# Performance work log

Hardware: AMD Instinct MI355X
Metric: run time of the kernel (lower is better)

The kernel has to match this reference:

```python
import jax, jax.numpy as jnp
import numpy as np

N, E = 50000, 1600000
IN_CH, HEADS, OUT_PER_HEAD = 128, 4, 32  # out_channels=128 // 4 heads
NEG_SLOPE = 0.2


def setup_inputs() -> dict:
    key = jax.random.key(0)
    ks = jax.random.split(key, 10)
    HC = HEADS * OUT_PER_HEAD
    glorot = lambda k, shape: jax.random.uniform(k, shape, jnp.float32, -1.0, 1.0) * jnp.sqrt(6.0 / (shape[0] + shape[-1]))
    return {
        "x": jax.random.normal(ks[0], (N, IN_CH), jnp.float32),
        "edge_index": jax.random.randint(ks[1], (2, E), 0, N),
        "edge_weight": jax.random.uniform(ks[2], (E,), jnp.float32),
        "Wl": glorot(ks[3], (IN_CH, HC)),
        "bl": jnp.zeros((HC,), jnp.float32),
        "Wr": glorot(ks[4], (IN_CH, HC)),
        "br": jnp.zeros((HC,), jnp.float32),
        "We": glorot(ks[5], (1, HC)),           # lin_edge, bias=False
        "att": glorot(ks[6], (HEADS, OUT_PER_HEAD)),
        "bias": jnp.zeros((HC,), jnp.float32),
    }


def reference(x, edge_index, edge_weight, Wl, bl, Wr, br, We, att, bias):
    n = x.shape[0]
    H, C = att.shape
    src, dst = edge_index[0], edge_index[1]
    # add_self_loops with fill_value='max': self-loop edge_attr = max incoming edge weight per node (0 if none)
    loop_attr = jax.ops.segment_max(edge_weight, dst, num_segments=n)
    loop_attr = jnp.where(jnp.isfinite(loop_attr), loop_attr, 0.0)
    loop = jnp.arange(n)
    src_f = jnp.concatenate([src, loop])
    dst_f = jnp.concatenate([dst, loop])
    ea_f = jnp.concatenate([edge_weight, loop_attr])[:, None]  # [E+N, 1]
    # GATv2: separate src/dst linear transforms
    x_l = (x @ Wl + bl).reshape(n, H, C)
    x_r = (x @ Wr + br).reshape(n, H, C)
    e = (ea_f @ We).reshape(-1, H, C)
    # per-edge message and attention score
    m = jax.nn.leaky_relu(x_l[src_f] + x_r[dst_f] + e, NEG_SLOPE)  # [E+N, H, C]
    alpha = jnp.einsum('ehc,hc->eh', m, att)
    # scatter-softmax over incoming edges per destination node
    amax = jax.ops.segment_max(alpha, dst_f, num_segments=n)
    amax = jnp.where(jnp.isfinite(amax), amax, 0.0)
    aexp = jnp.exp(alpha - amax[dst_f])
    asum = jax.ops.segment_sum(aexp, dst_f, num_segments=n)
    alpha = aexp / (asum[dst_f] + 1e-16)
    # weighted aggregate of source-transformed features
    out = jax.ops.segment_sum(x_l[src_f] * alpha[..., None], dst_f, num_segments=n)
    return out.reshape(n, H * C) + bias
```

## Files before the change

kernel.cpp:

```cpp
#include <hip/hip_runtime.h>
#include <cstdint>

#define NEG 0.2f
#define BSH 4
#define BNODES 16
#define CAP 768
#define EPT 3
#define SBSH 9
#define SBN 512
#define CCAP 18000
#define CCHUNK 3328
#define CEPT 13
#define LOG2E 1.44269504088896f

typedef __attribute__((ext_vector_type(8))) short short8v;
typedef __attribute__((ext_vector_type(4))) float f32x4;

__device__ __forceinline__ unsigned short f2bf(float f) {
  unsigned u = __float_as_uint(f);
  return (unsigned short)((u + 0x7FFFu + ((u >> 16) & 1u)) >> 16);
}

__global__ __launch_bounds__(256) void k_prep(const float* __restrict__ Wl,
    const float* __restrict__ Wr, unsigned short* __restrict__ WtB) {
  int mat = blockIdx.x;
  const float* W = mat ? Wr : Wl;
  for (int i = threadIdx.x; i < 16384; i += 256) {
    int c = i >> 7, k = i & 127;
    WtB[mat * 16384 + c * 128 + k] = f2bf(W[k * 128 + c]);
  }
}

__global__ __launch_bounds__(256) void k_gemm(const float* __restrict__ x,
    const unsigned short* __restrict__ WtB,
    const float* __restrict__ bl, const float* __restrict__ br,
    unsigned short* __restrict__ xlb, unsigned short* __restrict__ xrb, int n) {
  __shared__ __align__(16) unsigned short xs[64][136];
  __shared__ __align__(16) unsigned short Wt[128][136];
  int tid = threadIdx.x;
  int B0 = blockIdx.x * 64;
  int mat = blockIdx.y;
  for (int i = tid; i < 64 * 32; i += 256) {
    int r = i >> 5, c4 = (i & 31) * 4;
    ushort4 o = {0, 0, 0, 0};
    if (B0 + r < n) {
      float4 v = *(const float4*)(x + (size_t)(B0 + r) * 128 + c4);
      o = make_ushort4(f2bf(v.x), f2bf(v.y), f2bf(v.z), f2bf(v.w));
    }
    *(ushort4*)&xs[r][c4] = o;
  }
  for (int i = tid; i < 128 * 32; i += 256) {
    int c = i >> 5, k4 = (i & 31) * 4;
    *(ushort4*)&Wt[c][k4] = *(const ushort4*)(WtB + (size_t)mat * 16384 + c * 128 + k4);
  }
  __syncthreads();
  int wv = tid >> 6, lane = tid & 63;
  int l15 = lane & 15, g = lane >> 4;
  int R0 = wv * 16;
  f32x4 acc[8];
  #pragma unroll
  for (int t = 0; t < 8; ++t) acc[t] = {0.f, 0.f, 0.f, 0.f};
  #pragma unroll
  for (int kc = 0; kc < 4; ++kc) {
    int k0 = kc * 32 + g * 8;
    short8v b = *(const short8v*)&xs[R0 + l15][k0];
    #pragma unroll
    for (int t = 0; t < 8; ++t) {
      short8v a = *(const short8v*)&Wt[t * 16 + l15][k0];
      acc[t] = __builtin_amdgcn_mfma_f32_16x16x32_bf16(a, b, acc[t], 0, 0, 0);
    }
  }
  const float* bias = mat ? br : bl;
  unsigned short* yp = mat ? xrb : xlb;
  int row = B0 + R0 + l15;
  if (row < n) {
    #pragma unroll
    for (int t = 0; t < 8; ++t) {
      int c0 = t * 16 + g * 4;
      float4 bv = *(const float4*)(bias + c0);
      ushort4 o = {f2bf(acc[t][0] + bv.x), f2bf(acc[t][1] + bv.y),
                   f2bf(acc[t][2] + bv.z), f2bf(acc[t][3] + bv.w)};
      *(ushort4*)(yp + (size_t)row * 128 + c0) = o;
    }
  }
}

__global__ __launch_bounds__(256) void k_coarse(const int* __restrict__ eidx,
    const float* __restrict__ ew, unsigned* __restrict__ gsb,
    int2* __restrict__ csb, int E, int NSB) {
  __shared__ unsigned cnt[128];
  __shared__ unsigned base[128];
  int c0 = blockIdx.x * CCHUNK;
  int c1 = min(E, c0 + CCHUNK);
  if (c0 >= c1) return;
  for (int b = threadIdx.x; b < NSB; b += 256) cnt[b] = 0u;
  __syncthreads();
  unsigned dreg[CEPT];
  #pragma unroll
  for (int k = 0; k < CEPT; ++k) {
    int i = c0 + threadIdx.x + k * 256;
    unsigned d = 0u;
    if (i < c1) {
      d = (unsigned)eidx[E + i];
      atomicAdd(&cnt[d >> SBSH], 1u);
    }
    dreg[k] = d;
  }
  __syncthreads();
  for (int b = threadIdx.x; b < NSB; b += 256) {
    unsigned c = cnt[b];
    base[b] = c ? atomicAdd(&gsb[b], c) : 0u;
    cnt[b] = 0u;
  }
  __syncthreads();
  #pragma unroll
  for (int k = 0; k < CEPT; ++k) {
    int i = c0 + threadIdx.x + k * 256;
    if (i < c1) {
      unsigned d = dreg[k];
      unsigned b = d >> SBSH;
      unsigned slot = base[b] + atomicAdd(&cnt[b], 1u);
      if (slot < CCAP)
        csb[(size_t)b * CCAP + slot] =
            make_int2((eidx[i] << SBSH) | (int)(d & (SBN - 1)), __float_as_int(ew[i]));
    }
  }
}

__global__ __launch_bounds__(1024) void k_fine(const unsigned* __restrict__ gsb,
    const int2* __restrict__ csb, int2* __restrict__ ebkt,
    unsigned* __restrict__ fcnt, int NB) {
  __shared__ unsigned cnt[32];
  int sb = blockIdx.x;
  int ne = min((int)gsb[sb], CCAP);
  const int2* src = csb + (size_t)sb * CCAP;
  if (threadIdx.x < 32) cnt[threadIdx.x] = 0u;
  __syncthreads();
  for (int i = threadIdx.x; i < ne; i += 1024) {
    int2 e = src[i];
    int fb = (e.x >> 4) & 31;
    unsigned slot = atomicAdd(&cnt[fb], 1u);
    if (slot < CAP) {
      int packed = ((e.x >> SBSH) << 4) | (e.x & 15);
      ebkt[(size_t)(sb * 32 + fb) * CAP + slot] = make_int2(packed, e.y);
    }
  }
  __syncthreads();
  if (threadIdx.x < 32) {
    int fb = sb * 32 + (int)threadIdx.x;
    if (fb < NB) fcnt[fb] = min(cnt[threadIdx.x], (unsigned)CAP);
  }
}

__global__ __launch_bounds__(256) void k_agg(
    const unsigned* __restrict__ fcnt, const int2* __restrict__ ebkt,
    const unsigned short* __restrict__ xlb, const unsigned short* __restrict__ xrb,
    const float* __restrict__ We, const float* __restrict__ att,
    const float* __restrict__ bias, float* __restrict__ out, int n) {
  __shared__ int2 es[CAP];
  __shared__ unsigned rp[BNODES + 1];
  __shared__ unsigned cur[BNODES];
  __shared__ unsigned scnt[BNODES];
  int tid = threadIdx.x;
  int lane = tid & 63, wv = tid >> 6;
  int bkt = blockIdx.x;
  int ne = min((int)fcnt[bkt], CAP);
  const int2* srcp = ebkt + (size_t)bkt * CAP;
  if (tid < BNODES) scnt[tid] = 0u;
  __syncthreads();
  int2 er[EPT];
  #pragma unroll
  for (int k = 0; k < EPT; ++k) {
    int i = tid + k * 256;
    if (i < ne) {
      er[k] = srcp[i];
      atomicAdd(&scnt[er[k].x & (BNODES - 1)], 1u);
    }
  }
  __syncthreads();
  if (tid < 64) {
    unsigned s = (lane < BNODES) ? scnt[lane] : 0u;
    #pragma unroll
    for (int off = 1; off < BNODES; off <<= 1) {
      unsigned t = __shfl_up(s, off);
      if (lane >= off) s += t;
    }
    if (lane < BNODES) { rp[lane + 1] = s; cur[lane] = 0u; }
    if (lane == 0) rp[0] = 0u;
  }
  __syncthreads();
  #pragma unroll
  for (int k = 0; k < EPT; ++k) {
    int i = tid + k * 256;
    if (i < ne) {
      int dl = er[k].x & (BNODES - 1);
      unsigned slot = rp[dl] + atomicAdd(&cur[dl], 1u);
      es[slot] = make_int2(er[k].x >> BSH, er[k].y);
    }
  }
  __syncthreads();

  int g = lane >> 4;
  int l4 = lane & 15;
  int ch0 = l4 * 8;
  float4 weA = *(const float4*)(We + ch0);
  float4 weB = *(const float4*)(We + ch0 + 4);
  float4 atA = *(const float4*)(att + ch0);
  float4 atB = *(const float4*)(att + ch0 + 4);
  atA.x *= LOG2E; atA.y *= LOG2E; atA.z *= LOG2E; atA.w *= LOG2E;
  atB.x *= LOG2E; atB.y *= LOG2E; atB.z *= LOG2E; atB.w *= LOG2E;

  for (int dl = wv; dl < BNODES; dl += 4) {
    int d = (bkt << BSH) + dl;
    if (d >= n) break;
    int s0 = (int)rp[dl], s1 = (int)rp[dl + 1];
    uint4 xrq = *(const uint4*)(xrb + ((size_t)d << 7) + ch0);
    float4 xrA, xrB;
    xrA.x = __uint_as_float(xrq.x << 16);
    xrA.y = __uint_as_float(xrq.x & 0xFFFF0000u);
    xrA.z = __uint_as_float(xrq.y << 16);
    xrA.w = __uint_as_float(xrq.y & 0xFFFF0000u);
    xrB.x = __uint_as_float(xrq.z << 16);
    xrB.y = __uint_as_float(xrq.z & 0xFFFF0000u);
    xrB.z = __uint_as_float(xrq.w << 16);
    xrB.w = __uint_as_float(xrq.w & 0xFFFF0000u);
    float den = 0.f, wmax = -INFINITY;
    float4 aA = {0, 0, 0, 0}, aB = {0, 0, 0, 0};
    int idx = s0 + g;
    bool valid = idx < s1;
    int2 ev = make_int2(0, 0);
    uint4 xq = {0, 0, 0, 0};
    if (valid) {
      ev = es[idx];
      xq = *(const uint4*)(xlb + ((size_t)ev.x << 7) + ch0);
    }
    for (int j = s0; j < s1; j += 4) {
      int idxn = j + 4 + g;
      bool vn = idxn < s1;
      int2 evn = ev; uint4 xqn = xq;
      if (vn) {
        evn = es[idxn];
        xqn = *(const uint4*)(xlb + ((size_t)evn.x << 7) + ch0);
      }
      if (valid) {
        float w = __int_as_float(ev.y);
        wmax = fmaxf(wmax, w);
        float4 xA, xB;
        xA.x = __uint_as_float(xq.x << 16);
        xA.y = __uint_as_float(xq.x & 0xFFFF0000u);
        xA.z = __uint_as_float(xq.y << 16);
        xA.w = __uint_as_float(xq.y & 0xFFFF0000u);
        xB.x = __uint_as_float(xq.z << 16);
        xB.y = __uint_as_float(xq.z & 0xFFFF0000u);
        xB.z = __uint_as_float(xq.w << 16);
        xB.w = __uint_as_float(xq.w & 0xFFFF0000u);
        float4 tA, tB;
        tA.x = xA.x + xrA.x + w * weA.x;
        tA.y = xA.y + xrA.y + w * weA.y;
        tA.z = xA.z + xrA.z + w * weA.z;
        tA.w = xA.w + xrA.w + w * weA.w;
        tB.x = xB.x + xrB.x + w * weB.x;
        tB.y = xB.y + xrB.y + w * weB.y;
        tB.z = xB.z + xrB.z + w * weB.z;
        tB.w = xB.w + xrB.w + w * weB.w;
        tA.x = fmaxf(tA.x, NEG * tA.x);
        tA.y = fmaxf(tA.y, NEG * tA.y);
        tA.z = fmaxf(tA.z, NEG * tA.z);
        tA.w = fmaxf(tA.w, NEG * tA.w);
        tB.x = fmaxf(tB.x, NEG * tB.x);
        tB.y = fmaxf(tB.y, NEG * tB.y);
        tB.z = fmaxf(tB.z, NEG * tB.z);
        tB.w = fmaxf(tB.w, NEG * tB.w);
        float p = tA.x * atA.x + tA.y * atA.y + tA.z * atA.z + tA.w * atA.w
                + tB.x * atB.x + tB.y * atB.y + tB.z * atB.z + tB.w * atB.w;
        p += __shfl_xor(p, 1);
        p += __shfl_xor(p, 2);
        float pe = exp2f(p);
        den += pe;
        aA.x += pe * xA.x; aA.y += pe * xA.y; aA.z += pe * xA.z; aA.w += pe * xA.w;
        aB.x += pe * xB.x; aB.y += pe * xB.y; aB.z += pe * xB.z; aB.w += pe * xB.w;
      }
      ev = evn; xq = xqn; valid = vn;
    }
    #pragma unroll
    for (int mask = 16; mask <= 32; mask <<= 1) {
      den += __shfl_xor(den, mask);
      aA.x += __shfl_xor(aA.x, mask); aA.y += __shfl_xor(aA.y, mask);
      aA.z += __shfl_xor(aA.z, mask); aA.w += __shfl_xor(aA.w, mask);
      aB.x += __shfl_xor(aB.x, mask); aB.y += __shfl_xor(aB.y, mask);
      aB.z += __shfl_xor(aB.z, mask); aB.w += __shfl_xor(aB.w, mask);
      wmax = fmaxf(wmax, __shfl_xor(wmax, mask));
    }
    {
      float wl = (wmax > -INFINITY) ? wmax : 0.f;
      uint4 xq2 = *(const uint4*)(xlb + ((size_t)d << 7) + ch0);
      float4 xA, xB;
      xA.x = __uint_as_float(xq2.x << 16);
      xA.y = __uint_as_float(xq2.x & 0xFFFF0000u);
      xA.z = __uint_as_float(xq2.y << 16);
      xA.w = __uint_as_float(xq2.y & 0xFFFF0000u);
      xB.x = __uint_as_float(xq2.z << 16);
      xB.y = __uint_as_float(xq2.z & 0xFFFF0000u);
      xB.z = __uint_as_float(xq2.w << 16);
      xB.w = __uint_as_float(xq2.w & 0xFFFF0000u);
      float4 tA, tB;
      tA.x = xA.x + xrA.x + wl * weA.x;
      tA.y = xA.y + xrA.y + wl * weA.y;
      tA.z = xA.z + xrA.z + wl * weA.z;
      tA.w = xA.w + xrA.w + wl * weA.w;
      tB.x = xB.x + xrB.x + wl * weB.x;
      tB.y = xB.y + xrB.y + wl * weB.y;
      tB.z = xB.z + xrB.z + wl * weB.z;
      tB.w = xB.w + xrB.w + wl * weB.w;
      tA.x = fmaxf(tA.x, NEG * tA.x);
      tA.y = fmaxf(tA.y, NEG * tA.y);
      tA.z = fmaxf(tA.z, NEG * tA.z);
      tA.w = fmaxf(tA.w, NEG * tA.w);
      tB.x = fmaxf(tB.x, NEG * tB.x);
      tB.y = fmaxf(tB.y, NEG * tB.y);
      tB.z = fmaxf(tB.z, NEG * tB.z);
      tB.w = fmaxf(tB.w, NEG * tB.w);
      float p = tA.x * atA.x + tA.y * atA.y + tA.z * atA.z + tA.w * atA.w
              + tB.x * atB.x + tB.y * atB.y + tB.z * atB.z + tB.w * atB.w;
      p += __shfl_xor(p, 1);
      p += __shfl_xor(p, 2);
      float pe = exp2f(p);
      den += pe;
      aA.x += pe * xA.x; aA.y += pe * xA.y; aA.z += pe * xA.z; aA.w += pe * xA.w;
      aB.x += pe * xB.x; aB.y += pe * xB.y; aB.z += pe * xB.z; aB.w += pe * xB.w;
    }
    if (g == 0) {
      float r = 1.0f / den;
      float4 bvA = *(const float4*)(bias + ch0);
      float4 bvB = *(const float4*)(bias + ch0 + 4);
      float* op = out + (size_t)d * 128 + ch0;
      float4 oA = {aA.x * r + bvA.x, aA.y * r + bvA.y, aA.z * r + bvA.z, aA.w * r + bvA.w};
      float4 oB = {aB.x * r + bvB.x, aB.y * r + bvB.y, aB.z * r + bvB.z, aB.w * r + bvB.w};
      *(float4*)op = oA;
      *(float4*)(op + 4) = oB;
    }
  }
}

extern "C" void kernel_launch(void* const* d_in, const int* in_sizes, int n_in,
                              void* d_out, int out_size, void* d_ws, size_t ws_size,
                              hipStream_t stream) {
  const float* x     = (const float*)d_in[0];
  const int*   eidx  = (const int*)d_in[1];
  const float* ew_in = (const float*)d_in[2];
  const float* Wl    = (const float*)d_in[3];
  const float* bl    = (const float*)d_in[4];
  const float* Wr    = (const float*)d_in[5];
  const float* br    = (const float*)d_in[6];
  const float* We    = (const float*)d_in[7];
  const float* att   = (const float*)d_in[8];
  const float* bias  = (const float*)d_in[9];
  float* out = (float*)d_out;

  const int N = in_sizes[0] / 128;
  const int E = in_sizes[2];
  const int NB = (N + BNODES - 1) >> BSH;
  const int NSB = (N + SBN - 1) >> SBSH;

  char* ws = (char*)d_ws;
  size_t off = 0;
  auto alloc = [&](size_t bytes) {
    void* p = ws + off;
    off = (off + bytes + 255) & ~(size_t)255;
    return p;
  };
  int2* ebkt = (int2*)alloc((size_t)NB * CAP * 8);
  size_t ov_start = off;
  unsigned short* xlb = (unsigned short*)alloc((size_t)N * 128 * 2);
  unsigned short* xrb = (unsigned short*)alloc((size_t)N * 128 * 2);
  int2* csb = (int2*)(ws + ov_start);
  unsigned short* WtB = (unsigned short*)alloc(2 * 16384 * 2);
  unsigned* fcnt = (unsigned*)alloc((size_t)NB * 4);
  unsigned* gsb  = (unsigned*)alloc((size_t)NSB * 4);

  hipMemsetAsync(gsb, 0, (size_t)NSB * 4, stream);

  k_prep<<<2, 256, 0, stream>>>(Wl, Wr, WtB);

  int nblk = (E + CCHUNK - 1) / CCHUNK;
  k_coarse<<<nblk, 256, 0, stream>>>(eidx, ew_in, gsb, csb, E, NSB);

  k_fine<<<NSB, 1024, 0, stream>>>(gsb, csb, ebkt, fcnt, NB);

  k_gemm<<<dim3((N + 63) / 64, 2), 256, 0, stream>>>(x, WtB, bl, br, xlb, xrb, N);

  k_agg<<<NB, 256, 0, stream>>>(fcnt, ebkt, xlb, xrb, We, att, bias, out, N);
}
```

Baseline: 165.3 us.

## Decompose leaky-relu attention into linear terms plus abs and split fine bucketing

Rewrites leaky_relu(t)·att as 0.6·att·t + 0.4·att·|t|. The linear part is precomputed per node in the GEMM epilogue (ql, qr) and per head for the edge weight (qe), so the per-edge loop only needs an fma+abs chain instead of max and multiply. Separately, k_fine is split into 8 slices per super-bucket using two-pass counting with global atomic bases to raise parallelism. Costs are extra per-node scalar loads and memsetting fcnt, plus small numerical differences because the linear part is computed from bf16-rounded features.

Measured after the change: 162.6 us. No clear change (-1.7%).

```diff
diff --git a/kernel.cpp b/kernel.cpp
--- a/kernel.cpp
+++ b/kernel.cpp
@@ -11,6 +11,7 @@
 #define CCAP 18000
 #define CCHUNK 3328
 #define CEPT 13
+#define FSLICE 8
 #define LOG2E 1.44269504088896f
 
 typedef __attribute__((ext_vector_type(8))) short short8v;
@@ -20,21 +21,37 @@
   unsigned u = __float_as_uint(f);
   return (unsigned short)((u + 0x7FFFu + ((u >> 16) & 1u)) >> 16);
 }
+__device__ __forceinline__ float bf2f(unsigned short h) {
+  return __uint_as_float(((unsigned)h) << 16);
+}
 
 __global__ __launch_bounds__(256) void k_prep(const float* __restrict__ Wl,
-    const float* __restrict__ Wr, unsigned short* __restrict__ WtB) {
+    const float* __restrict__ Wr, const float* __restrict__ We,
+    const float* __restrict__ att, unsigned short* __restrict__ WtB,
+    float* __restrict__ qe) {
   int mat = blockIdx.x;
   const float* W = mat ? Wr : Wl;
   for (int i = threadIdx.x; i < 16384; i += 256) {
     int c = i >> 7, k = i & 127;
     WtB[mat * 16384 + c * 128 + k] = f2bf(W[k * 128 + c]);
   }
+  if (mat == 0) {
+    __shared__ float tmp[128];
+    if (threadIdx.x < 128) tmp[threadIdx.x] = att[threadIdx.x] * We[threadIdx.x];
+    __syncthreads();
+    if (threadIdx.x < 4) {
+      float s = 0.f;
+      for (int c = 0; c < 32; ++c) s += tmp[threadIdx.x * 32 + c];
+      qe[threadIdx.x] = 0.6f * LOG2E * s;
+    }
+  }
 }
 
 __global__ __launch_bounds__(256) void k_gemm(const float* __restrict__ x,
-    const unsigned short* __restrict__ WtB,
+    const unsigned short* __restrict__ WtB, const float* __restrict__ att,
     const float* __restrict__ bl, const float* __restrict__ br,
-    unsigned short* __restrict__ xlb, unsigned short* __restrict__ xrb, int n) {
+    unsigned short* __restrict__ xlb, unsigned short* __restrict__ xrb,
+    float* __restrict__ ql, float* __restrict__ qr, int n) {
   __shared__ __align__(16) unsigned short xs[64][136];
   __shared__ __align__(16) unsigned short Wt[128][136];
   int tid = threadIdx.x;
@@ -72,17 +89,31 @@
   }
   const float* bias = mat ? br : bl;
   unsigned short* yp = mat ? xrb : xlb;
+  float* qdst = mat ? qr : ql;
   int row = B0 + R0 + l15;
+  float qp[4] = {0.f, 0.f, 0.f, 0.f};
   if (row < n) {
+    const float s06 = 0.6f * LOG2E;
     #pragma unroll
     for (int t = 0; t < 8; ++t) {
       int c0 = t * 16 + g * 4;
       float4 bv = *(const float4*)(bias + c0);
+      float4 av = *(const float4*)(att + c0);
       ushort4 o = {f2bf(acc[t][0] + bv.x), f2bf(acc[t][1] + bv.y),
                    f2bf(acc[t][2] + bv.z), f2bf(acc[t][3] + bv.w)};
       *(ushort4*)(yp + (size_t)row * 128 + c0) = o;
-    }
-  }
+      float dot = av.x * bf2f(o.x) + av.y * bf2f(o.y)
+                + av.z * bf2f(o.z) + av.w * bf2f(o.w);
+      qp[t >> 1] += s06 * dot;
+    }
+  }
+  #pragma unroll
+  for (int h = 0; h < 4; ++h) {
+    qp[h] += __shfl_xor(qp[h], 16);
+    qp[h] += __shfl_xor(qp[h], 32);
+  }
+  if (row < n && g == 0)
+    *(float4*)(qdst + (size_t)row * 4) = make_float4(qp[0], qp[1], qp[2], qp[3]);
 }
 
 __global__ __launch_bounds__(256) void k_coarse(const int* __restrict__ eidx,
@@ -127,36 +158,47 @@
   }
 }
 
-__global__ __launch_bounds__(1024) void k_fine(const unsigned* __restrict__ gsb,
+__global__ __launch_bounds__(256) void k_fine(const unsigned* __restrict__ gsb,
     const int2* __restrict__ csb, int2* __restrict__ ebkt,
     unsigned* __restrict__ fcnt, int NB) {
   __shared__ unsigned cnt[32];
-  int sb = blockIdx.x;
+  __shared__ unsigned base[32];
+  int sb = blockIdx.x / FSLICE;
+  int sl = blockIdx.x % FSLICE;
   int ne = min((int)gsb[sb], CCAP);
+  int chunk = (ne + FSLICE - 1) / FSLICE;
+  int i0 = sl * chunk, i1 = min(ne, i0 + chunk);
+  if (i0 >= i1) return;
   const int2* src = csb + (size_t)sb * CCAP;
   if (threadIdx.x < 32) cnt[threadIdx.x] = 0u;
   __syncthreads();
-  for (int i = threadIdx.x; i < ne; i += 1024) {
+  for (int i = i0 + threadIdx.x; i < i1; i += 256)
+    atomicAdd(&cnt[(src[i].x >> 4) & 31], 1u);
+  __syncthreads();
+  if (threadIdx.x < 32) {
+    unsigned c = cnt[threadIdx.x];
+    base[threadIdx.x] = c ? atomicAdd(&fcnt[sb * 32 + (int)threadIdx.x], c) : 0u;
+    cnt[threadIdx.x] = 0u;
+  }
+  __syncthreads();
+  for (int i = i0 + threadIdx.x; i < i1; i += 256) {
     int2 e = src[i];
     int fb = (e.x >> 4) & 31;
-    unsigned slot = atomicAdd(&cnt[fb], 1u);
+    unsigned slot = base[fb] + atomicAdd(&cnt[fb], 1u);
     if (slot < CAP) {
       int packed = ((e.x >> SBSH) << 4) | (e.x & 15);
       ebkt[(size_t)(sb * 32 + fb) * CAP + slot] = make_int2(packed, e.y);
     }
   }
-  __syncthreads();
-  if (threadIdx.x < 32) {
-    int fb = sb * 32 + (int)threadIdx.x;
-    if (fb < NB) fcnt[fb] = min(cnt[threadIdx.x], (unsigned)CAP);
-  }
 }
 
 __global__ __launch_bounds__(256) void k_agg(
     const unsigned* __restrict__ fcnt, const int2* __restrict__ ebkt,
     const unsigned short* __restrict__ xlb, const unsigned short* __restrict__ xrb,
-    const float* __restrict__ We, const float* __restrict__ att,
-    const float* __restrict__ bias, float* __restrict__ out, int n) {
+    const float* __restrict__ ql, const float* __restrict__ qr,
+    const float* __restrict__ qe, const float* __restrict__ We,
+    const float* __restrict__ att, const float* __restrict__ bias,
+    float* __restrict__ out, int n) {
   __shared__ int2 es[CAP];
   __shared__ unsigned rp[BNODES + 1];
   __shared__ unsigned cur[BNODES];
@@ -202,13 +244,16 @@
 
   int g = lane >> 4;
   int l4 = lane & 15;
+  int h = l4 >> 2;
   int ch0 = l4 * 8;
   float4 weA = *(const float4*)(We + ch0);
   float4 weB = *(const float4*)(We + ch0 + 4);
   float4 atA = *(const float4*)(att + ch0);
   float4 atB = *(const float4*)(att + ch0 + 4);
-  atA.x *= LOG2E; atA.y *= LOG2E; atA.z *= LOG2E; atA.w *= LOG2E;
-  atB.x *= LOG2E; atB.y *= LOG2E; atB.z *= LOG2E; atB.w *= LOG2E;
+  const float s04 = 0.4f * LOG2E;
+  atA.x *= s04; atA.y *= s04; atA.z *= s04; atA.w *= s04;
+  atB.x *= s04; atB.y *= s04; atB.z *= s04; atB.w *= s04;
+  float qeh = qe[h];
 
   for (int dl = wv; dl < BNODES; dl += 4) {
     int d = (bkt << BSH) + dl;
@@ -224,23 +269,27 @@
     xrB.y = __uint_as_float(xrq.z & 0xFFFF0000u);
     xrB.z = __uint_as_float(xrq.w << 16);
     xrB.w = __uint_as_float(xrq.w & 0xFFFF0000u);
+    float qrd = qr[(size_t)d * 4 + h];
     float den = 0.f, wmax = -INFINITY;
     float4 aA = {0, 0, 0, 0}, aB = {0, 0, 0, 0};
     int idx = s0 + g;
     bool valid = idx < s1;
     int2 ev = make_int2(0, 0);
     uint4 xq = {0, 0, 0, 0};
+    float qls = 0.f;
     if (valid) {
       ev = es[idx];
       xq = *(const uint4*)(xlb + ((size_t)ev.x << 7) + ch0);
+      qls = ql[(size_t)ev.x * 4 + h];
     }
     for (int j = s0; j < s1; j += 4) {
       int idxn = j + 4 + g;
       bool vn = idxn < s1;
-      int2 evn = ev; uint4 xqn = xq;
+      int2 evn = ev; uint4 xqn = xq; float qln = qls;
       if (vn) {
         evn = es[idxn];
         xqn = *(const uint4*)(xlb + ((size_t)evn.x << 7) + ch0);
+        qln = ql[(size_t)evn.x * 4 + h];
       }
       if (valid) {
         float w = __int_as_float(ev.y);
@@ -254,33 +303,23 @@
         xB.y = __uint_as_float(xq.z & 0xFFFF0000u);
         xB.z = __uint_as_float(xq.w << 16);
         xB.w = __uint_as_float(xq.w & 0xFFFF0000u);
-        float4 tA, tB;
-        tA.x = xA.x + xrA.x + w * weA.x;
-        tA.y = xA.y + xrA.y + w * weA.y;
-        tA.z = xA.z + xrA.z + w * weA.z;
-        tA.w = xA.w + xrA.w + w * weA.w;
-        tB.x = xB.x + xrB.x + w * weB.x;
-        tB.y = xB.y + xrB.y + w * weB.y;
-        tB.z = xB.z + xrB.z + w * weB.z;
-        tB.w = xB.w + xrB.w + w * weB.w;
-        tA.x = fmaxf(tA.x, NEG * tA.x);
-        tA.y = fmaxf(tA.y, NEG * tA.y);
-        tA.z = fmaxf(tA.z, NEG * tA.z);
-        tA.w = fmaxf(tA.w, NEG * tA.w);
-        tB.x = fmaxf(tB.x, NEG * tB.x);
-        tB.y = fmaxf(tB.y, NEG * tB.y);
-        tB.z = fmaxf(tB.z, NEG * tB.z);
-        tB.w = fmaxf(tB.w, NEG * tB.w);
-        float p = tA.x * atA.x + tA.y * atA.y + tA.z * atA.z + tA.w * atA.w
-                + tB.x * atB.x + tB.y * atB.y + tB.z * atB.z + tB.w * atB.w;
-        p += __shfl_xor(p, 1);
-        p += __shfl_xor(p, 2);
-        float pe = exp2f(p);
+        float nl = 0.f, t;
+        t = xA.x + fmaf(w, weA.x, xrA.x); nl = fmaf(atA.x, fabsf(t), nl);
+        t = xA.y + fmaf(w, weA.y, xrA.y); nl = fmaf(atA.y, fabsf(t), nl);
+        t = xA.z + fmaf(w, weA.z, xrA.z); nl = fmaf(atA.z, fabsf(t), nl);
+        t = xA.w + fmaf(w, weA.w, xrA.w); nl = fmaf(atA.w, fabsf(t), nl);
+        t = xB.x + fmaf(w, weB.x, xrB.x); nl = fmaf(atB.x, fabsf(t), nl);
+        t = xB.y + fmaf(w, weB.y, xrB.y); nl = fmaf(atB.y, fabsf(t), nl);
+        t = xB.z + fmaf(w, weB.z, xrB.z); nl = fmaf(atB.z, fabsf(t), nl);
+        t = xB.w + fmaf(w, weB.w, xrB.w); nl = fmaf(atB.w, fabsf(t), nl);
+        nl += __shfl_xor(nl, 1);
+        nl += __shfl_xor(nl, 2);
+        float pe = exp2f(qls + fmaf(w, qeh, qrd) + nl);
         den += pe;
         aA.x += pe * xA.x; aA.y += pe * xA.y; aA.z += pe * xA.z; aA.w += pe * xA.w;
         aB.x += pe * xB.x; aB.y += pe * xB.y; aB.z += pe * xB.z; aB.w += pe * xB.w;
       }
-      ev = evn; xq = xqn; valid = vn;
+      ev = evn; xq = xqn; qls = qln; valid = vn;
     }
     #pragma unroll
     for (int mask = 16; mask <= 32; mask <<= 1) {
@@ -303,28 +342,19 @@
       xB.y = __uint_as_float(xq2.z & 0xFFFF0000u);
       xB.z = __uint_as_float(xq2.w << 16);
       xB.w = __uint_as_float(xq2.w & 0xFFFF0000u);
-      float4 tA, tB;
-      tA.x = xA.x + xrA.x + wl * weA.x;
-      tA.y = xA.y + xrA.y + wl * weA.y;
-      tA.z = xA.z + xrA.z + wl * weA.z;
-      tA.w = xA.w + xrA.w + wl * weA.w;
-      tB.x = xB.x + xrB.x + wl * weB.x;
-      tB.y = xB.y + xrB.y + wl * weB.y;
-      tB.z = xB.z + xrB.z + wl * weB.z;
-      tB.w = xB.w + xrB.w + wl * weB.w;
-      tA.x = fmaxf(tA.x, NEG * tA.x);
-      tA.y = fmaxf(tA.y, NEG * tA.y);
-      tA.z = fmaxf(tA.z, NEG * tA.z);
-      tA.w = fmaxf(tA.w, NEG * tA.w);
-      tB.x = fmaxf(tB.x, NEG * tB.x);
-      tB.y = fmaxf(tB.y, NEG * tB.y);
-      tB.z = fmaxf(tB.z, NEG * tB.z);
-      tB.w = fmaxf(tB.w, NEG * tB.w);
-      float p = tA.x * atA.x + tA.y * atA.y + tA.z * atA.z + tA.w * atA.w
-              + tB.x * atB.x + tB.y * atB.y + tB.z * atB.z + tB.w * atB.w;
-      p += __shfl_xor(p, 1);
-      p += __shfl_xor(p, 2);
-      float pe = exp2f(p);
+      float nl = 0.f, t;
+      t = xA.x + fmaf(wl, weA.x, xrA.x); nl = fmaf(atA.x, fabsf(t), nl);
+      t = xA.y + fmaf(wl, weA.y, xrA.y); nl = fmaf(atA.y, fabsf(t), nl);
+      t = xA.z + fmaf(wl, weA.z, xrA.z); nl = fmaf(atA.z, fabsf(t), nl);
+      t = xA.w + fmaf(wl, weA.w, xrA.w); nl = fmaf(atA.w, fabsf(t), nl);
+      t = xB.x + fmaf(wl, weB.x, xrB.x); nl = fmaf(atB.x, fabsf(t), nl);
+      t = xB.y + fmaf(wl, weB.y, xrB.y); nl = fmaf(atB.y, fabsf(t), nl);
+      t = xB.z + fmaf(wl, weB.z, xrB.z); nl = fmaf(atB.z, fabsf(t), nl);
+      t = xB.w + fmaf(wl, weB.w, xrB.w); nl = fmaf(atB.w, fabsf(t), nl);
+      nl += __shfl_xor(nl, 1);
+      nl += __shfl_xor(nl, 2);
+      float qld = ql[(size_t)d * 4 + h];
+      float pe = exp2f(qld + fmaf(wl, qeh, qrd) + nl);
       den += pe;
       aA.x += pe * xA.x; aA.y += pe * xA.y; aA.z += pe * xA.z; aA.w += pe * xA.w;
       aB.x += pe * xB.x; aB.y += pe * xB.y; aB.z += pe * xB.z; aB.w += pe * xB.w;
@@ -375,19 +405,24 @@
   unsigned short* xrb = (unsigned short*)alloc((size_t)N * 128 * 2);
   int2* csb = (int2*)(ws + ov_start);
   unsigned short* WtB = (unsigned short*)alloc(2 * 16384 * 2);
+  float* ql = (float*)alloc((size_t)N * 4 * 4);
+  float* qr = (float*)alloc((size_t)N * 4 * 4);
+  float* qe = (float*)alloc(4 * 4);
   unsigned* fcnt = (unsigned*)alloc((size_t)NB * 4);
   unsigned* gsb  = (unsigned*)alloc((size_t)NSB * 4);
 
-  hipMemsetAsync(gsb, 0, (size_t)NSB * 4, stream);
-
-  k_prep<<<2, 256, 0, stream>>>(Wl, Wr, WtB);
+  size_t z0 = (size_t)((char*)fcnt - ws);
+  size_t z1 = (size_t)((char*)gsb - ws) + (size_t)NSB * 4;
+  hipMemsetAsync(ws + z0, 0, z1 - z0, stream);
+
+  k_prep<<<2, 256, 0, stream>>>(Wl, Wr, We, att, WtB, qe);
 
   int nblk = (E + CCHUNK - 1) / CCHUNK;
   k_coarse<<<nblk, 256, 0, stream>>>(eidx, ew_in, gsb, csb, E, NSB);
 
-  k_fine<<<NSB, 1024, 0, stream>>>(gsb, csb, ebkt, fcnt, NB);
-
-  k_gemm<<<dim3((N + 63) / 64, 2), 256, 0, stream>>>(x, WtB, bl, br, xlb, xrb, N);
-
-  k_agg<<<NB, 256, 0, stream>>>(fcnt, ebkt, xlb, xrb, We, att, bias, out, N);
-}
+  k_fine<<<NSB * FSLICE, 256, 0, stream>>>(gsb, csb, ebkt, fcnt, NB);
+
+  k_gemm<<<dim3((N + 63) / 64, 2), 256, 0, stream>>>(x, WtB, att, bl, br, xlb, xrb, ql, qr, N);
+
+  k_agg<<<NB, 256, 0, stream>>>(fcnt, ebkt, xlb, xrb, ql, qr, qe, We, att, bias, out, N);
+}
```
